# Optimization experiments

Measured on AMD Instinct MI355X. Metric: run time of the kernel, lower is better.

Reference implementation:

```python
import jax, jax.numpy as jnp
import numpy as np

NEG_INF = -10000.0


def setup_inputs() -> dict:
    key = jax.random.key(0)
    ks = jax.random.split(key, 8)
    B, S, H, V, NU, MV = 32, 256, 768, 30522, 5, 4
    f = lambda k, shape, s=1.0: jax.random.normal(k, shape, dtype=jnp.float32) * s
    return dict(
        input_ids=jax.random.randint(ks[0], (B, S), 0, V),
        decoder_inputs=f(ks[1], (B, NU, H)),
        encoder_output=f(ks[2], (B, S, H)),
        hidden=f(ks[3], (1, B, H)),
        embed_weight=f(ks[4], (V, H), 0.02),
        gru_w_ih=f(ks[5], (3 * H, H), 0.02),
        gru_w_hh=f(ks[6], (3 * H, H), 0.02),
        gru_b_ih=jnp.zeros((3 * H,), jnp.float32),
        gru_b_hh=jnp.zeros((3 * H,), jnp.float32),
        wgen_w=f(ks[7], (1, 3 * H), 0.02),
        wgen_b=jnp.zeros((1,), jnp.float32),
        max_value=MV,
    )


def reference(input_ids, decoder_inputs, encoder_output, hidden, embed_weight,
              gru_w_ih, gru_w_hh, gru_b_ih, gru_b_hh, wgen_w, wgen_b, max_value):
    B, S = input_ids.shape
    V, H = embed_weight.shape
    mask = (input_ids == 0)                      # [B,S] pad mask
    rows = jnp.arange(B)[:, None]                # for batched scatter-add

    def gru_cell(x, h):                          # PyTorch GRU, gate order r,z,n
        gi = x @ gru_w_ih.T + gru_b_ih
        gh = h @ gru_w_hh.T + gru_b_hh
        i_r, i_z, i_n = jnp.split(gi, 3, axis=-1)
        h_r, h_z, h_n = jnp.split(gh, 3, axis=-1)
        r = jax.nn.sigmoid(i_r + h_r)
        z = jax.nn.sigmoid(i_z + h_z)
        n = jnp.tanh(i_n + r * h_n)
        return (1.0 - z) * n + z * h

    def inner(carry, _):
        w, h = carry                             # w: [B,H] current input token emb
        h = gru_cell(w, h)                       # [B,H]
        attn_e = jnp.einsum('bsh,bh->bs', encoder_output, h)
        attn_hist = jax.nn.softmax(jnp.where(mask, NEG_INF, attn_e), axis=-1)  # [B,S]
        attn_vocab = jax.nn.softmax(h @ embed_weight.T, axis=-1)               # [B,V]
        context = jnp.einsum('bs,bsh->bh', attn_hist, encoder_output)          # [B,H]
        p_gen = jax.nn.sigmoid(
            jnp.concatenate([w, h, context], axis=-1) @ wgen_w.T + wgen_b)     # [B,1]
        # pointer distribution: scatter attention mass onto vocab ids
        p_ptr = jnp.zeros((B, V), attn_vocab.dtype).at[rows, input_ids].add(attn_hist)
        p_final = p_gen * attn_vocab + (1.0 - p_gen) * p_ptr                   # [B,V]
        w_idx = jnp.argmax(p_final, axis=-1)                                   # greedy
        return (embed_weight[w_idx], h), p_final

    def outer(h, w0):                            # w0: [B,H] slot query embedding
        (_, h), p = jax.lax.scan(inner, (w0, h), None, length=max_value)
        return h, p                              # p: [max_value,B,V]

    h0 = hidden[0]                               # [B,H]
    _, outs = jax.lax.scan(outer, h0, jnp.swapaxes(decoder_inputs, 0, 1))
    # outs: [n_update, max_value, B, V] -> [B, n_update, max_value, V]
    return jnp.transpose(outs, (2, 0, 1, 3))
```

## Files before the change

### kernel.cpp

```cpp
#include <hip/hip_runtime.h>
#include <math.h>

#define B 32
#define S 256
#define H 768
#define V 30522
#define NU 5
#define MV 4
#define NEG_INF -10000.0f

__device__ __forceinline__ float sigm(float x){ return 1.0f/(1.0f + expf(-x)); }

__global__ __launch_bounds__(256) void gru_kernel(
    const float* __restrict__ wp, int wstride,
    const float* __restrict__ hin, float* __restrict__ hout,
    const float* __restrict__ Wih, const float* __restrict__ Whh,
    const float* __restrict__ bih, const float* __restrict__ bhh)
{
    int wid  = blockIdx.x * 4 + (threadIdx.x >> 6);
    int lane = threadIdx.x & 63;
    int j  = wid >> 2;
    int bg = wid & 3;

    float aI0[8], aI1[8], aI2[8], aH0[8], aH1[8], aH2[8];
#pragma unroll
    for (int bb = 0; bb < 8; bb++){ aI0[bb]=aI1[bb]=aI2[bb]=aH0[bb]=aH1[bb]=aH2[bb]=0.f; }

#pragma unroll
    for (int it = 0; it < 3; it++){
        int k = it*256 + lane*4;
        float4 w0 = *(const float4*)(Wih + (size_t)(0*H + j)*H + k);
        float4 w1 = *(const float4*)(Wih + (size_t)(1*H + j)*H + k);
        float4 w2 = *(const float4*)(Wih + (size_t)(2*H + j)*H + k);
        float4 u0 = *(const float4*)(Whh + (size_t)(0*H + j)*H + k);
        float4 u1 = *(const float4*)(Whh + (size_t)(1*H + j)*H + k);
        float4 u2 = *(const float4*)(Whh + (size_t)(2*H + j)*H + k);
#pragma unroll
        for (int bb = 0; bb < 8; bb++){
            int b = bg*8 + bb;
            float4 x = *(const float4*)(wp  + (size_t)b*wstride + k);
            float4 h = *(const float4*)(hin + (size_t)b*H + k);
            aI0[bb] += w0.x*x.x + w0.y*x.y + w0.z*x.z + w0.w*x.w;
            aI1[bb] += w1.x*x.x + w1.y*x.y + w1.z*x.z + w1.w*x.w;
            aI2[bb] += w2.x*x.x + w2.y*x.y + w2.z*x.z + w2.w*x.w;
            aH0[bb] += u0.x*h.x + u0.y*h.y + u0.z*h.z + u0.w*h.w;
            aH1[bb] += u1.x*h.x + u1.y*h.y + u1.z*h.z + u1.w*h.w;
            aH2[bb] += u2.x*h.x + u2.y*h.y + u2.z*h.z + u2.w*h.w;
        }
    }
    float rRZ0[8], rRZ1[8], rIN[8], rHN[8];
#pragma unroll
    for (int bb = 0; bb < 8; bb++){
        rRZ0[bb] = aI0[bb] + aH0[bb];
        rRZ1[bb] = aI1[bb] + aH1[bb];
        rIN[bb]  = aI2[bb];
        rHN[bb]  = aH2[bb];
    }
#pragma unroll
    for (int bb = 0; bb < 8; bb++){
#pragma unroll
        for (int m = 32; m >= 1; m >>= 1){
            rRZ0[bb] += __shfl_xor(rRZ0[bb], m, 64);
            rRZ1[bb] += __shfl_xor(rRZ1[bb], m, 64);
            rIN[bb]  += __shfl_xor(rIN[bb],  m, 64);
            rHN[bb]  += __shfl_xor(rHN[bb],  m, 64);
        }
    }
    if (lane == 0){
        float brz0 = bih[j]     + bhh[j];
        float brz1 = bih[H+j]   + bhh[H+j];
        float bin_ = bih[2*H+j];
        float bhn_ = bhh[2*H+j];
#pragma unroll
        for (int bb = 0; bb < 8; bb++){
            int b = bg*8 + bb;
            float r = sigm(rRZ0[bb] + brz0);
            float z = sigm(rRZ1[bb] + brz1);
            float n = tanhf(rIN[bb] + bin_ + r*(rHN[bb] + bhn_));
            float ho = hin[(size_t)b*H + j];
            hout[(size_t)b*H + j] = (1.0f - z)*n + z*ho;
        }
    }
}

__global__ __launch_bounds__(256) void attn_e_kernel(
    const float* __restrict__ hb, const float* __restrict__ enc,
    float* __restrict__ attnE)
{
    int wid  = blockIdx.x * 4 + (threadIdx.x >> 6);
    int lane = threadIdx.x & 63;
    int b = wid >> 8;
    int s = wid & 255;
    const float* er = enc + ((size_t)b*S + s)*H;
    const float* hr = hb + (size_t)b*H;
    float acc = 0.f;
#pragma unroll
    for (int it = 0; it < 3; it++){
        int k = it*256 + lane*4;
        float4 e4 = *(const float4*)(er + k);
        float4 h4 = *(const float4*)(hr + k);
        acc += e4.x*h4.x + e4.y*h4.y + e4.z*h4.z + e4.w*h4.w;
    }
#pragma unroll
    for (int m = 32; m >= 1; m >>= 1) acc += __shfl_xor(acc, m, 64);
    if (lane == 0) attnE[b*S + s] = acc;
}

__global__ __launch_bounds__(256) void ctx_kernel(
    const float* __restrict__ attnE, const int* __restrict__ ids,
    const float* __restrict__ enc, float* __restrict__ attnH,
    float* __restrict__ ctx)
{
    __shared__ float ah[S];
    __shared__ float red[S];
    int b  = blockIdx.x / 3;
    int kc = blockIdx.x % 3;
    int t  = threadIdx.x;

    float e = attnE[b*S + t];
    if (ids[b*S + t] == 0) e = NEG_INF;
    red[t] = e; __syncthreads();
    for (int s = 128; s > 0; s >>= 1){ if (t < s) red[t] = fmaxf(red[t], red[t+s]); __syncthreads(); }
    float mx = red[0]; __syncthreads();
    float p = expf(e - mx);
    red[t] = p; __syncthreads();
    for (int s = 128; s > 0; s >>= 1){ if (t < s) red[t] += red[t+s]; __syncthreads(); }
    float a = p / red[0];
    ah[t] = a;
    if (kc == 0) attnH[b*S + t] = a;
    __syncthreads();

    int k = kc*256 + t;
    const float* ep = enc + (size_t)b*S*H + k;
    float acc = 0.f;
#pragma unroll 4
    for (int s = 0; s < S; s++) acc += ah[s] * ep[(size_t)s*H];
    ctx[b*H + k] = acc;
}

#define LK 384
#define HSTRIDE 388
__global__ __launch_bounds__(1024) void logits_kernel(
    const float* __restrict__ hb, const float* __restrict__ E,
    float* __restrict__ logits,
    const float* __restrict__ wp, int wstride,
    const float* __restrict__ ctx, const float* __restrict__ wgw,
    const float* __restrict__ wgb, float* __restrict__ pgen)
{
    __shared__ float sh[32 * HSTRIDE];
    int t = threadIdx.x;

    if (blockIdx.x == 239){
        int b = t >> 5, sl = t & 31;
        float s = 0.f;
        for (int i = sl; i < 2304; i += 32){
            float xv;
            if (i < 768)        xv = wp[(size_t)b*wstride + i];
            else if (i < 1536)  xv = hb[b*H + (i - 768)];
            else                xv = ctx[b*H + (i - 1536)];
            s += xv * wgw[i];
        }
#pragma unroll
        for (int m = 16; m >= 1; m >>= 1) s += __shfl_xor(s, m, 32);
        if (sl == 0) pgen[b] = sigm(s + wgb[0]);
        return;
    }

    int lane = t & 63;
    int w    = t >> 6;
    int b    = lane & 31;
    int vh   = lane >> 5;
    int v0   = blockIdx.x*128 + w*8 + vh*4;

    float acc0 = 0.f, acc1 = 0.f, acc2 = 0.f, acc3 = 0.f;

    for (int ph = 0; ph < 2; ph++){
        __syncthreads();
        for (int i = t; i < 32*LK; i += 1024){
            int bb = i / LK; int c = i - bb*LK;
            sh[bb*HSTRIDE + c] = hb[bb*H + ph*LK + c];
        }
        __syncthreads();
        const float* hrow = sh + b*HSTRIDE;
        if (v0 + 3 < V){
            const float* e0 = E + (size_t)(v0+0)*H + ph*LK;
            const float* e1 = E + (size_t)(v0+1)*H + ph*LK;
            const float* e2 = E + (size_t)(v0+2)*H + ph*LK;
            const float* e3 = E + (size_t)(v0+3)*H + ph*LK;
            for (int k = 0; k < LK; k += 4){
                float4 h4 = *(const float4*)(hrow + k);
                float4 a4 = *(const float4*)(e0 + k);
                float4 b4 = *(const float4*)(e1 + k);
                float4 c4 = *(const float4*)(e2 + k);
                float4 d4 = *(const float4*)(e3 + k);
                acc0 += h4.x*a4.x + h4.y*a4.y + h4.z*a4.z + h4.w*a4.w;
                acc1 += h4.x*b4.x + h4.y*b4.y + h4.z*b4.z + h4.w*b4.w;
                acc2 += h4.x*c4.x + h4.y*c4.y + h4.z*c4.z + h4.w*c4.w;
                acc3 += h4.x*d4.x + h4.y*d4.y + h4.z*d4.z + h4.w*d4.w;
            }
        } else {
#pragma unroll
            for (int jj = 0; jj < 4; jj++){
                int v = v0 + jj;
                if (v < V){
                    const float* ev = E + (size_t)v*H + ph*LK;
                    float a = 0.f;
                    for (int k = 0; k < LK; k += 4){
                        float4 h4 = *(const float4*)(hrow + k);
                        float4 e4 = *(const float4*)(ev + k);
                        a += h4.x*e4.x + h4.y*e4.y + h4.z*e4.z + h4.w*e4.w;
                    }
                    if (jj == 0) acc0 += a; else if (jj == 1) acc1 += a;
                    else if (jj == 2) acc2 += a; else acc3 += a;
                }
            }
        }
    }
    if (v0 + 0 < V) logits[(size_t)b*V + v0 + 0] = acc0;
    if (v0 + 1 < V) logits[(size_t)b*V + v0 + 1] = acc1;
    if (v0 + 2 < V) logits[(size_t)b*V + v0 + 2] = acc2;
    if (v0 + 3 < V) logits[(size_t)b*V + v0 + 3] = acc3;
}

__global__ __launch_bounds__(1024) void vred_kernel(
    const float* __restrict__ logits, float* __restrict__ vmax, float* __restrict__ vsum)
{
    __shared__ float red[1024];
    int b = blockIdx.x, t = threadIdx.x;
    float r[30]; int n = 0;
    float mx = -INFINITY;
    for (int i = t; i < V; i += 1024){
        float x = logits[(size_t)b*V + i];
        r[n++] = x;
        mx = fmaxf(mx, x);
    }
    red[t] = mx; __syncthreads();
    for (int s = 512; s > 0; s >>= 1){ if (t < s) red[t] = fmaxf(red[t], red[t+s]); __syncthreads(); }
    mx = red[0]; __syncthreads();
    float sm = 0.f;
    for (int i = 0; i < n; i++) sm += expf(r[i] - mx);
    red[t] = sm; __syncthreads();
    for (int s = 512; s > 0; s >>= 1){ if (t < s) red[t] += red[t+s]; __syncthreads(); }
    if (t == 0){ vmax[b] = mx; vsum[b] = red[0]; }
}

__global__ __launch_bounds__(1024) void final_kernel(
    const float* __restrict__ logits, const float* __restrict__ vmax,
    const float* __restrict__ vsum, const float* __restrict__ pgen,
    float* __restrict__ out, int u, int mm)
{
    int b = blockIdx.y;
    int v = blockIdx.x*1024 + threadIdx.x;
    if (v >= V) return;
    float val = pgen[b] * expf(logits[(size_t)b*V + v] - vmax[b]) / vsum[b];
    out[(((size_t)b*NU + u)*MV + mm)*(size_t)V + v] = val;
}

__global__ __launch_bounds__(256) void scatter_kernel(
    const float* __restrict__ attnH, const int* __restrict__ ids,
    const float* __restrict__ pgen, float* __restrict__ out, int u, int mm)
{
    int b = blockIdx.x, s = threadIdx.x;
    int id = ids[b*S + s];
    float val = (1.0f - pgen[b]) * attnH[b*S + s];
    atomicAdd(out + (((size_t)b*NU + u)*MV + mm)*(size_t)V + id, val);
}

__global__ __launch_bounds__(1024) void argmax_kernel(
    const float* __restrict__ out, int u, int mm,
    const float* __restrict__ E, float* __restrict__ wbuf)
{
    __shared__ float rv[1024];
    __shared__ int   ri[1024];
    int b = blockIdx.x, t = threadIdx.x;
    const float* row = out + (((size_t)b*NU + u)*MV + mm)*(size_t)V;
    float bv = -INFINITY; int bi = 0;
    for (int i = t; i < V; i += 1024){
        float x = row[i];
        if (x > bv){ bv = x; bi = i; }
    }
    rv[t] = bv; ri[t] = bi; __syncthreads();
    for (int s = 512; s > 0; s >>= 1){
        if (t < s){
            if (rv[t+s] > rv[t] || (rv[t+s] == rv[t] && ri[t+s] < ri[t])){
                rv[t] = rv[t+s]; ri[t] = ri[t+s];
            }
        }
        __syncthreads();
    }
    int idx = ri[0];
    for (int k = t; k < H; k += 1024) wbuf[b*H + k] = E[(size_t)idx*H + k];
}

extern "C" void kernel_launch(void* const* d_in, const int* in_sizes, int n_in,
                              void* d_out, int out_size, void* d_ws, size_t ws_size,
                              hipStream_t stream)
{
    const int*   ids = (const int*)  d_in[0];
    const float* dec = (const float*)d_in[1];
    const float* enc = (const float*)d_in[2];
    const float* hid = (const float*)d_in[3];
    const float* E   = (const float*)d_in[4];
    const float* Wih = (const float*)d_in[5];
    const float* Whh = (const float*)d_in[6];
    const float* bih = (const float*)d_in[7];
    const float* bhh = (const float*)d_in[8];
    const float* wgw = (const float*)d_in[9];
    const float* wgb = (const float*)d_in[10];
    float* out = (float*)d_out;
    float* ws  = (float*)d_ws;

    float* wbuf    = ws;
    float* hb0     = ws + 24576;
    float* hb1     = ws + 49152;
    float* ctxb    = ws + 73728;
    float* attnE   = ws + 98304;
    float* attnH   = ws + 106496;
    float* logitsb = ws + 114688;
    float* pgenb   = ws + 1091392;
    float* vmaxb   = ws + 1091424;
    float* vsumb   = ws + 1091456;

    for (int u = 0; u < NU; u++){
        for (int mm = 0; mm < MV; mm++){
            int st = u*MV + mm;
            const float* wp; int wstride;
            if (mm == 0){ wp = dec + (size_t)u*H; wstride = NU*H; }
            else        { wp = wbuf;              wstride = H; }
            const float* hin = (st == 0) ? hid : ((st & 1) ? hb0 : hb1);
            float*      hout = (st & 1) ? hb1 : hb0;

            gru_kernel<<<768, 256, 0, stream>>>(wp, wstride, hin, hout, Wih, Whh, bih, bhh);
            attn_e_kernel<<<2048, 256, 0, stream>>>(hout, enc, attnE);
            ctx_kernel<<<96, 256, 0, stream>>>(attnE, ids, enc, attnH, ctxb);
            logits_kernel<<<240, 1024, 0, stream>>>(hout, E, logitsb, wp, wstride, ctxb, wgw, wgb, pgenb);
            vred_kernel<<<32, 1024, 0, stream>>>(logitsb, vmaxb, vsumb);
            final_kernel<<<dim3(30, 32), 1024, 0, stream>>>(logitsb, vmaxb, vsumb, pgenb, out, u, mm);
            scatter_kernel<<<32, 256, 0, stream>>>(attnH, ids, pgenb, out, u, mm);
            if (mm != MV-1)
                argmax_kernel<<<32, 1024, 0, stream>>>(out, u, mm, E, wbuf);
        }
    }
}
```

Baseline: 3.890 ms.

## Retile vocab logits GEMM with LDS-staged embedding tiles and split-K partials

New measurement: 3.417 ms. 12.1% less time.

```diff
diff --git a/kernel.cpp b/kernel.cpp
--- a/kernel.cpp
+++ b/kernel.cpp
@@ -9,11 +9,19 @@
 #define MV 4
 #define NEG_INF -10000.0f
 
+#define VP 30720
+#define KSPLIT 4
+#define KCH 192
+#define KT 32
+#define VT 256
+#define VPAD 260
+
 __device__ __forceinline__ float sigm(float x){ return 1.0f/(1.0f + expf(-x)); }
 
 __global__ __launch_bounds__(256) void gru_kernel(
     const float* __restrict__ wp, int wstride,
     const float* __restrict__ hin, float* __restrict__ hout,
+    float* __restrict__ htr,
     const float* __restrict__ Wih, const float* __restrict__ Whh,
     const float* __restrict__ bih, const float* __restrict__ bhh)
 {
@@ -78,7 +86,9 @@
             float z = sigm(rRZ1[bb] + brz1);
             float n = tanhf(rIN[bb] + bin_ + r*(rHN[bb] + bhn_));
             float ho = hin[(size_t)b*H + j];
-            hout[(size_t)b*H + j] = (1.0f - z)*n + z*ho;
+            float hv = (1.0f - z)*n + z*ho;
+            hout[(size_t)b*H + j] = hv;
+            htr[(size_t)j*32 + b] = hv;
         }
     }
 }
@@ -138,22 +148,19 @@
     ctx[b*H + k] = acc;
 }
 
-#define LK 384
-#define HSTRIDE 388
-__global__ __launch_bounds__(1024) void logits_kernel(
-    const float* __restrict__ hb, const float* __restrict__ E,
-    float* __restrict__ logits,
-    const float* __restrict__ wp, int wstride,
+__global__ __launch_bounds__(256) void logits_kernel(
+    const float* __restrict__ E, const float* __restrict__ htr,
+    float* __restrict__ part,
+    const float* __restrict__ hb, const float* __restrict__ wp, int wstride,
     const float* __restrict__ ctx, const float* __restrict__ wgw,
     const float* __restrict__ wgb, float* __restrict__ pgen)
 {
-    __shared__ float sh[32 * HSTRIDE];
     int t = threadIdx.x;
 
-    if (blockIdx.x == 239){
-        int b = t >> 5, sl = t & 31;
+    if (blockIdx.x == 480){
+        int b = t >> 3, sl = t & 7;
         float s = 0.f;
-        for (int i = sl; i < 2304; i += 32){
+        for (int i = sl; i < 2304; i += 8){
             float xv;
             if (i < 768)        xv = wp[(size_t)b*wstride + i];
             else if (i < 1536)  xv = hb[b*H + (i - 768)];
@@ -161,76 +168,78 @@
             s += xv * wgw[i];
         }
 #pragma unroll
-        for (int m = 16; m >= 1; m >>= 1) s += __shfl_xor(s, m, 32);
+        for (int m = 4; m >= 1; m >>= 1) s += __shfl_xor(s, m, 8);
         if (sl == 0) pgen[b] = sigm(s + wgb[0]);
         return;
     }
 
-    int lane = t & 63;
-    int w    = t >> 6;
-    int b    = lane & 31;
-    int vh   = lane >> 5;
-    int v0   = blockIdx.x*128 + w*8 + vh*4;
-
-    float acc0 = 0.f, acc1 = 0.f, acc2 = 0.f, acc3 = 0.f;
-
-    for (int ph = 0; ph < 2; ph++){
+    __shared__ float Ets[KT][VPAD];
+    int vt = blockIdx.x >> 2;
+    int ks = blockIdx.x & 3;
+    int v0 = vt * VT;
+    int k0 = ks * KCH;
+
+    int wu = __builtin_amdgcn_readfirstlane(t >> 6);
+    int l  = t & 63;
+    int r  = t >> 3;
+    int c4 = t & 7;
+
+    float4 acc[8];
+#pragma unroll
+    for (int j = 0; j < 8; j++){ acc[j].x=0.f; acc[j].y=0.f; acc[j].z=0.f; acc[j].w=0.f; }
+
+    for (int ph = 0; ph < KCH/KT; ph++){
+        int kb = k0 + ph*KT;
         __syncthreads();
-        for (int i = t; i < 32*LK; i += 1024){
-            int bb = i / LK; int c = i - bb*LK;
-            sh[bb*HSTRIDE + c] = hb[bb*H + ph*LK + c];
+#pragma unroll
+        for (int p = 0; p < 8; p++){
+            int vv = v0 + p*32 + r;
+            int vr = vv < V ? vv : V-1;
+            float4 e4 = *(const float4*)(E + (size_t)vr*H + kb + c4*4);
+            int vloc = p*32 + r;
+            Ets[c4*4+0][vloc] = e4.x;
+            Ets[c4*4+1][vloc] = e4.y;
+            Ets[c4*4+2][vloc] = e4.z;
+            Ets[c4*4+3][vloc] = e4.w;
         }
         __syncthreads();
-        const float* hrow = sh + b*HSTRIDE;
-        if (v0 + 3 < V){
-            const float* e0 = E + (size_t)(v0+0)*H + ph*LK;
-            const float* e1 = E + (size_t)(v0+1)*H + ph*LK;
-            const float* e2 = E + (size_t)(v0+2)*H + ph*LK;
-            const float* e3 = E + (size_t)(v0+3)*H + ph*LK;
-            for (int k = 0; k < LK; k += 4){
-                float4 h4 = *(const float4*)(hrow + k);
-                float4 a4 = *(const float4*)(e0 + k);
-                float4 b4 = *(const float4*)(e1 + k);
-                float4 c4 = *(const float4*)(e2 + k);
-                float4 d4 = *(const float4*)(e3 + k);
-                acc0 += h4.x*a4.x + h4.y*a4.y + h4.z*a4.z + h4.w*a4.w;
-                acc1 += h4.x*b4.x + h4.y*b4.y + h4.z*b4.z + h4.w*b4.w;
-                acc2 += h4.x*c4.x + h4.y*c4.y + h4.z*c4.z + h4.w*c4.w;
-                acc3 += h4.x*d4.x + h4.y*d4.y + h4.z*d4.z + h4.w*d4.w;
-            }
-        } else {
-#pragma unroll
-            for (int jj = 0; jj < 4; jj++){
-                int v = v0 + jj;
-                if (v < V){
-                    const float* ev = E + (size_t)v*H + ph*LK;
-                    float a = 0.f;
-                    for (int k = 0; k < LK; k += 4){
-                        float4 h4 = *(const float4*)(hrow + k);
-                        float4 e4 = *(const float4*)(ev + k);
-                        a += h4.x*e4.x + h4.y*e4.y + h4.z*e4.z + h4.w*e4.w;
-                    }
-                    if (jj == 0) acc0 += a; else if (jj == 1) acc1 += a;
-                    else if (jj == 2) acc2 += a; else acc3 += a;
-                }
-            }
-        }
-    }
-    if (v0 + 0 < V) logits[(size_t)b*V + v0 + 0] = acc0;
-    if (v0 + 1 < V) logits[(size_t)b*V + v0 + 1] = acc1;
-    if (v0 + 2 < V) logits[(size_t)b*V + v0 + 2] = acc2;
-    if (v0 + 3 < V) logits[(size_t)b*V + v0 + 3] = acc3;
+        const float* hkp = htr + (size_t)kb*32 + 8*wu;
+#pragma unroll
+        for (int k = 0; k < KT; k++){
+            float4 e4 = *(const float4*)(&Ets[k][l*4]);
+            float h0 = hkp[k*32+0], h1 = hkp[k*32+1], h2 = hkp[k*32+2], h3 = hkp[k*32+3];
+            float h4 = hkp[k*32+4], h5 = hkp[k*32+5], h6 = hkp[k*32+6], h7 = hkp[k*32+7];
+            acc[0].x += h0*e4.x; acc[0].y += h0*e4.y; acc[0].z += h0*e4.z; acc[0].w += h0*e4.w;
+            acc[1].x += h1*e4.x; acc[1].y += h1*e4.y; acc[1].z += h1*e4.z; acc[1].w += h1*e4.w;
+            acc[2].x += h2*e4.x; acc[2].y += h2*e4.y; acc[2].z += h2*e4.z; acc[2].w += h2*e4.w;
+            acc[3].x += h3*e4.x; acc[3].y += h3*e4.y; acc[3].z += h3*e4.z; acc[3].w += h3*e4.w;
+            acc[4].x += h4*e4.x; acc[4].y += h4*e4.y; acc[4].z += h4*e4.z; acc[4].w += h4*e4.w;
+            acc[5].x += h5*e4.x; acc[5].y += h5*e4.y; acc[5].z += h5*e4.z; acc[5].w += h5*e4.w;
+            acc[6].x += h6*e4.x; acc[6].y += h6*e4.y; acc[6].z += h6*e4.z; acc[6].w += h6*e4.w;
+            acc[7].x += h7*e4.x; acc[7].y += h7*e4.y; acc[7].z += h7*e4.z; acc[7].w += h7*e4.w;
+        }
+    }
+    float* pp = part + (size_t)ks*32*VP;
+    int v = v0 + l*4;
+#pragma unroll
+    for (int j = 0; j < 8; j++){
+        int b = 8*wu + j;
+        *(float4*)(pp + (size_t)b*VP + v) = acc[j];
+    }
 }
 
 __global__ __launch_bounds__(1024) void vred_kernel(
-    const float* __restrict__ logits, float* __restrict__ vmax, float* __restrict__ vsum)
+    const float* __restrict__ part, float* __restrict__ vmax, float* __restrict__ vsum)
 {
     __shared__ float red[1024];
     int b = blockIdx.x, t = threadIdx.x;
     float r[30]; int n = 0;
     float mx = -INFINITY;
     for (int i = t; i < V; i += 1024){
-        float x = logits[(size_t)b*V + i];
+        float x = part[(size_t)b*VP + i]
+                + part[(size_t)(32+b)*VP + i]
+                + part[(size_t)(64+b)*VP + i]
+                + part[(size_t)(96+b)*VP + i];
         r[n++] = x;
         mx = fmaxf(mx, x);
     }
@@ -245,14 +254,18 @@
 }
 
 __global__ __launch_bounds__(1024) void final_kernel(
-    const float* __restrict__ logits, const float* __restrict__ vmax,
+    const float* __restrict__ part, const float* __restrict__ vmax,
     const float* __restrict__ vsum, const float* __restrict__ pgen,
     float* __restrict__ out, int u, int mm)
 {
     int b = blockIdx.y;
     int v = blockIdx.x*1024 + threadIdx.x;
     if (v >= V) return;
-    float val = pgen[b] * expf(logits[(size_t)b*V + v] - vmax[b]) / vsum[b];
+    float x = part[(size_t)b*VP + v]
+            + part[(size_t)(32+b)*VP + v]
+            + part[(size_t)(64+b)*VP + v]
+            + part[(size_t)(96+b)*VP + v];
+    float val = pgen[b] * expf(x - vmax[b]) / vsum[b];
     out[(((size_t)b*NU + u)*MV + mm)*(size_t)V + v] = val;
 }
 
@@ -316,10 +329,11 @@
     float* ctxb    = ws + 73728;
     float* attnE   = ws + 98304;
     float* attnH   = ws + 106496;
-    float* logitsb = ws + 114688;
-    float* pgenb   = ws + 1091392;
-    float* vmaxb   = ws + 1091424;
-    float* vsumb   = ws + 1091456;
+    float* htr     = ws + 114688;
+    float* pgenb   = ws + 139264;
+    float* vmaxb   = ws + 139296;
+    float* vsumb   = ws + 139328;
+    float* part    = ws + 139360;
 
     for (int u = 0; u < NU; u++){
         for (int mm = 0; mm < MV; mm++){
@@ -330,12 +344,12 @@
             const float* hin = (st == 0) ? hid : ((st & 1) ? hb0 : hb1);
             float*      hout = (st & 1) ? hb1 : hb0;
 
-            gru_kernel<<<768, 256, 0, stream>>>(wp, wstride, hin, hout, Wih, Whh, bih, bhh);
+            gru_kernel<<<768, 256, 0, stream>>>(wp, wstride, hin, hout, htr, Wih, Whh, bih, bhh);
             attn_e_kernel<<<2048, 256, 0, stream>>>(hout, enc, attnE);
             ctx_kernel<<<96, 256, 0, stream>>>(attnE, ids, enc, attnH, ctxb);
-            logits_kernel<<<240, 1024, 0, stream>>>(hout, E, logitsb, wp, wstride, ctxb, wgw, wgb, pgenb);
-            vred_kernel<<<32, 1024, 0, stream>>>(logitsb, vmaxb, vsumb);
-            final_kernel<<<dim3(30, 32), 1024, 0, stream>>>(logitsb, vmaxb, vsumb, pgenb, out, u, mm);
+            logits_kernel<<<481, 256, 0, stream>>>(E, htr, part, hout, wp, wstride, ctxb, wgw, wgb, pgenb);
+            vred_kernel<<<32, 1024, 0, stream>>>(part, vmaxb, vsumb);
+            final_kernel<<<dim3(30, 32), 1024, 0, stream>>>(part, vmaxb, vsumb, pgenb, out, u, mm);
             scatter_kernel<<<32, 256, 0, stream>>>(attnH, ids, pgenb, out, u, mm);
             if (mm != MV-1)
                 argmax_kernel<<<32, 1024, 0, stream>>>(out, u, mm, E, wbuf);
```
